# Kernel optimization log

Measured on AMD Instinct MI355X. Metric: run time of the kernel, lower is better.

## Reference

```python
import jax, jax.numpy as jnp
import numpy as np
import math

DIM = 1024
NUM_HEADS = 16
HEAD_DIM = DIM // NUM_HEADS
ROPE_BASE = 10000.0


def _rope_cos_sin(seq_len, head_dim, dtype):
    inv_freq = 1.0 / (ROPE_BASE ** (jnp.arange(0, head_dim, 2, dtype=jnp.float32) / head_dim))
    t = jnp.arange(seq_len, dtype=jnp.float32)
    freqs = jnp.einsum('i,j->ij', t, inv_freq)          # (S, head_dim/2)
    emb = jnp.concatenate([freqs, freqs], axis=-1)      # (S, head_dim)
    return jnp.cos(emb).astype(dtype), jnp.sin(emb).astype(dtype)


def _rotate_half(x):
    x1, x2 = jnp.split(x, 2, axis=-1)
    return jnp.concatenate([-x2, x1], axis=-1)


def setup_inputs() -> dict:
    key = jax.random.key(0)
    kx, kq, kk, kv, ko = jax.random.split(key, 5)
    B, S = 4, 2048
    scale = 1.0 / math.sqrt(DIM)
    x = jax.random.normal(kx, (B, S, DIM), dtype=jnp.float32)
    Wq = jax.random.normal(kq, (DIM, DIM), dtype=jnp.float32) * scale
    Wk = jax.random.normal(kk, (DIM, DIM), dtype=jnp.float32) * scale
    Wv = jax.random.normal(kv, (DIM, DIM), dtype=jnp.float32) * scale
    Wo = jax.random.normal(ko, (DIM, DIM), dtype=jnp.float32) * scale
    mask = jnp.tril(jnp.ones((S, S), dtype=jnp.int32))  # causal mask
    return {"x": x, "Wq": Wq, "Wk": Wk, "Wv": Wv, "Wo": Wo, "mask": mask}


def reference(x, Wq, Wk, Wv, Wo, mask):
    B, S, _ = x.shape
    # projections (nn.Linear: y = x @ W.T)
    def split_heads(t):
        return t.reshape(B, S, NUM_HEADS, HEAD_DIM).transpose(0, 2, 1, 3)  # (B,H,S,D)
    q = split_heads(x @ Wq.T)
    k = split_heads(x @ Wk.T)
    v = split_heads(x @ Wv.T)
    # RoPE
    cos, sin = _rope_cos_sin(S, HEAD_DIM, x.dtype)      # (S, D)
    cos = cos[None, None]; sin = sin[None, None]
    q = q * cos + _rotate_half(q) * sin
    k = k * cos + _rotate_half(k) * sin
    # attention
    scores = jnp.einsum('bhsd,bhtd->bhst', q, k) / math.sqrt(HEAD_DIM)
    neg_inf = jnp.asarray(-jnp.inf, dtype=scores.dtype)
    scores = jnp.where(mask[None, None] == 0, neg_inf, scores)
    attn = jax.nn.softmax(scores, axis=-1)
    out = jnp.einsum('bhst,bhtd->bhsd', attn, v)        # (B,H,S,D)
    out = out.transpose(0, 2, 1, 3).reshape(B, S, DIM)
    return out @ Wo.T
```

## Files before the change

kernel.cpp:

```cpp
#include <hip/hip_runtime.h>
#include <hip/hip_bf16.h>

#define BDIM 1024
#define NH 16
#define HD 64
#define BB 4
#define SS 2048
#define MTOT (BB*SS)
#define NT (SS/64)

typedef __bf16 bf16x8 __attribute__((ext_vector_type(8)));
typedef float f32x4 __attribute__((ext_vector_type(4)));

__device__ __forceinline__ unsigned short f2b(float f){
    __bf16 h = (__bf16)f;
    return __builtin_bit_cast(unsigned short, h);
}

__device__ __forceinline__ unsigned cvtpk(float lo, float hi){
    unsigned u;
    asm("v_cvt_pk_bf16_f32 %0, %1, %2" : "=v"(u) : "v"(lo), "v"(hi));
    return u;
}

__device__ __forceinline__ void ld16(const unsigned short* g, unsigned short* l){
    __builtin_amdgcn_global_load_lds(
        (const __attribute__((address_space(1))) unsigned int*)(const void*)g,
        (__attribute__((address_space(3))) unsigned int*)(void*)l, 16, 0, 0);
}

__global__ void setup_all(const float* __restrict__ x,
                          const float* __restrict__ Wq, const float* __restrict__ Wk,
                          const float* __restrict__ Wv, const float* __restrict__ Wo,
                          unsigned short* __restrict__ xb,
                          unsigned short* __restrict__ oq, unsigned short* __restrict__ ok,
                          unsigned short* __restrict__ ov, unsigned short* __restrict__ oo,
                          float2* __restrict__ rt){
    const int bid = blockIdx.x;
    const int tid = threadIdx.x;
    if (bid < 8192){
        int i = bid * 256 + tid;
        float4 v = ((const float4*)x)[i];
        ushort4 o;
        o.x = f2b(v.x); o.y = f2b(v.y); o.z = f2b(v.z); o.w = f2b(v.w);
        ((ushort4*)xb)[i] = o;
    } else if (bid < 12288){
        int idx = bid - 8192;
        int which = idx >> 10;
        const float* in = (which == 0) ? Wq : (which == 1) ? Wk : (which == 2) ? Wv : Wo;
        unsigned short* out = (which == 0) ? oq : (which == 1) ? ok : (which == 2) ? ov : oo;
        int i = (idx & 1023) * 256 + tid;
        float4 v = ((const float4*)in)[i];
        ushort4 o;
        o.x = f2b(v.x); o.y = f2b(v.y); o.z = f2b(v.z); o.w = f2b(v.w);
        ((ushort4*)out)[i] = o;
    } else {
        int i = (bid - 12288) * 256 + tid;
        int s = i >> 5, d = i & 31;
        float theta = (float)s * exp2f(-0.41524101186092029f * (float)d);
        float sn, c;
        sincosf(theta, &sn, &c);
        rt[i] = make_float2(c, sn);
    }
}

__device__ __forceinline__ void gemm_mainloop(
    const unsigned short* __restrict__ A,
    const unsigned short* __restrict__ Bw,
    unsigned short* At, unsigned short* Bt,
    f32x4 acc[4][4], int m0, int n0)
{
    const int tid  = threadIdx.x;
    const int lane = tid & 63;
    const int wave = tid >> 6;
    const int wr = wave >> 1, wc = wave & 1;
    const int lh = lane >> 4, ll = lane & 15;
    const int K = 1024;

    for (int k0 = 0; k0 < K; k0 += 64){
        #pragma unroll
        for (int c = 0; c < 4; ++c){
            int g   = c*256 + tid;
            int row = g >> 3;
            int off = (g & 7) * 8;
            int base = (c*256 + wave*64) * 8;
            ld16(A  + (size_t)(m0+row)*K + k0 + off, At + base);
            ld16(Bw + (size_t)(n0+row)*K + k0 + off, Bt + base);
        }
        __syncthreads();
        #pragma unroll
        for (int ks = 0; ks < 2; ++ks){
            bf16x8 af[4], bfr[4];
            #pragma unroll
            for (int i = 0; i < 4; ++i)
                af[i] = *(const bf16x8*)(At + (wr*64 + i*16 + ll)*64 + ks*32 + lh*8);
            #pragma unroll
            for (int j = 0; j < 4; ++j)
                bfr[j] = *(const bf16x8*)(Bt + (wc*64 + j*16 + ll)*64 + ks*32 + lh*8);
            #pragma unroll
            for (int i = 0; i < 4; ++i)
                #pragma unroll
                for (int j = 0; j < 4; ++j)
                    acc[i][j] = __builtin_amdgcn_mfma_f32_16x16x32_bf16(af[i], bfr[j], acc[i][j], 0, 0, 0);
        }
        __syncthreads();
    }
}

#define TILE_US 4096

__global__ __launch_bounds__(256, 4) void gemm_qkv(
    const unsigned short* __restrict__ Xb,
    const unsigned short* __restrict__ Wq,
    const unsigned short* __restrict__ Wk,
    const unsigned short* __restrict__ Wv,
    const float2* __restrict__ Rt,
    unsigned short* __restrict__ Qt,
    unsigned short* __restrict__ Kt,
    unsigned short* __restrict__ VTt)
{
    __shared__ alignas(16) unsigned short At[128*64];
    __shared__ alignas(16) unsigned short Bt[128*64];
    const int z = blockIdx.z;
    const unsigned short* Bw = (z == 0) ? Wq : (z == 1 ? Wk : Wv);
    const int m0 = blockIdx.y * 128, n0 = blockIdx.x * 128;
    f32x4 acc[4][4] = {};
    gemm_mainloop(Xb, Bw, At, Bt, acc, m0, n0);

    const int lane = threadIdx.x & 63;
    const int wave = threadIdx.x >> 6;
    const int wr = wave >> 1, wc = wave & 1;
    const int lh = lane >> 4, ll = lane & 15;
    const int h  = blockIdx.x*2 + wc;
    const int b  = m0 >> 11;
    const int bh = b*NH + h;

    if (z < 2){
        const float qs = (z == 0) ? 0.125f * 1.44269504f : 1.0f;
        unsigned short* C = (z == 0) ? Qt : Kt;
        #pragma unroll
        for (int i = 0; i < 4; ++i)
            #pragma unroll
            for (int r = 0; r < 4; ++r){
                int m = m0 + wr*64 + i*16 + lh*4 + r;
                int s = m & (SS-1);
                int kt = s >> 6;
                const float2* rowcs = Rt + (s << 5);
                size_t fb = ((size_t)(bh*NT + kt)*8 + i)*512 + (size_t)(lh*4 + r)*8;
                #pragma unroll
                for (int jl = 0; jl < 2; ++jl){
                    int d_lo = jl*16 + ll;
                    float2 cs = rowcs[d_lo];
                    float a_lo = acc[i][jl][r], a_hi = acc[i][jl+2][r];
                    float y_lo = (a_lo*cs.x - a_hi*cs.y) * qs;
                    float y_hi = (a_hi*cs.x + a_lo*cs.y) * qs;
                    size_t off = fb + (size_t)(jl*2 + (ll>>3))*128 + (ll&7);
                    C[off]        = f2b(y_lo);
                    C[off + 2048] = f2b(y_hi);
                }
            }
    } else {
        const int s0 = (m0 & (SS-1)) + wr*64;
        const int kt = s0 >> 6;
        #pragma unroll
        for (int i = 0; i < 4; ++i)
            #pragma unroll
            for (int j = 0; j < 4; ++j){
                unsigned short tmp[4];
                #pragma unroll
                for (int r = 0; r < 4; ++r)
                    tmp[r] = f2b(acc[i][j][r]);
                size_t off = ((size_t)(bh*NT + kt)*8 + (i>>1)*4 + j)*512
                           + (size_t)(((i&1)*2 + (lh>>1))*16 + ll)*8 + (lh&1)*4;
                *(uint2*)(VTt + off) = *(const uint2*)tmp;
            }
    }
}

__global__ __launch_bounds__(256, 4) void gemm_out(
    const unsigned short* __restrict__ Ab,
    const unsigned short* __restrict__ Wo,
    float* __restrict__ Cout)
{
    __shared__ alignas(16) unsigned short At[128*64];
    __shared__ alignas(16) unsigned short Bt[128*64];
    const int m0 = blockIdx.y * 128, n0 = blockIdx.x * 128;
    f32x4 acc[4][4] = {};
    gemm_mainloop(Ab, Wo, At, Bt, acc, m0, n0);

    const int lane = threadIdx.x & 63;
    const int wave = threadIdx.x >> 6;
    const int wr = wave >> 1, wc = wave & 1;
    const int lh = lane >> 4, ll = lane & 15;
    #pragma unroll
    for (int i = 0; i < 4; ++i)
        #pragma unroll
        for (int j = 0; j < 4; ++j)
            #pragma unroll
            for (int r = 0; r < 4; ++r){
                int m = m0 + wr*64 + i*16 + lh*4 + r;
                int n = n0 + wc*64 + j*16 + ll;
                Cout[(size_t)m*BDIM + n] = acc[i][j][r];
            }
}

__device__ __forceinline__ void attn_tile(
    const bf16x8 qf[2], bool diag, int ws, int lane, int lh, int ll,
    const unsigned short* Ksh, const unsigned short* Vsh,
    float& li, f32x4 o[4])
{
    f32x4 sc[4] = {};
    #pragma unroll
    for (int ks = 0; ks < 2; ++ks)
        #pragma unroll
        for (int j = 0; j < 4; ++j){
            bf16x8 kfr = *(const bf16x8*)(Ksh + (ks*4 + j)*512 + lane*8);
            sc[j] = __builtin_amdgcn_mfma_f32_16x16x32_bf16(kfr, qf[ks], sc[j], 0, 0, 0);
        }
    if (diag){
        int qrow = ws*16 + ll;
        #pragma unroll
        for (int j = 0; j < 4; ++j)
            #pragma unroll
            for (int r = 0; r < 4; ++r)
                if (j*16 + lh*4 + r > qrow) sc[j][r] = -1e30f;
    }
    #pragma unroll
    for (int j = 0; j < 4; ++j)
        #pragma unroll
        for (int r = 0; r < 4; ++r)
            sc[j][r] = exp2f(sc[j][r] - 28.0f);
    float s = 0.f;
    #pragma unroll
    for (int j = 0; j < 4; ++j)
        s += (sc[j][0] + sc[j][1]) + (sc[j][2] + sc[j][3]);
    li += s;
    #pragma unroll
    for (int ks = 0; ks < 2; ++ks){
        unsigned a = cvtpk(sc[2*ks][0],   sc[2*ks][1]);
        unsigned b = cvtpk(sc[2*ks+1][0], sc[2*ks+1][1]);
        unsigned c = cvtpk(sc[2*ks][2],   sc[2*ks][3]);
        unsigned d = cvtpk(sc[2*ks+1][2], sc[2*ks+1][3]);
        asm("v_permlane32_swap_b32 %0, %1" : "+v"(a), "+v"(b));
        asm("v_permlane16_swap_b32 %0, %1" : "+v"(a), "+v"(b));
        asm("v_permlane32_swap_b32 %0, %1" : "+v"(c), "+v"(d));
        asm("v_permlane16_swap_b32 %0, %1" : "+v"(c), "+v"(d));
        uint4 uu = make_uint4(a, c, b, d);
        bf16x8 pf = __builtin_bit_cast(bf16x8, uu);
        #pragma unroll
        for (int t = 0; t < 4; ++t){
            bf16x8 vf = *(const bf16x8*)(Vsh + (ks*4 + t)*512 + lane*8);
            o[t] = __builtin_amdgcn_mfma_f32_16x16x32_bf16(pf, vf, o[t], 0, 0, 0);
        }
    }
}

__device__ __forceinline__ void store_o(
    unsigned short* S, const f32x4 o[4], const float li[4],
    int lane, int lh, int ll, int q0w, int b, int h,
    unsigned short* __restrict__ Obuf)
{
    #pragma unroll
    for (int r = 0; r < 4; ++r){
        float inv = 1.0f / li[r];
        #pragma unroll
        for (int t = 0; t < 4; ++t)
            S[(lh*4 + r)*72 + t*16 + ll] = f2b(o[t][r] * inv);
    }
    int row = lane >> 2, c4 = (lane & 3) * 8;
    size_t rb = ((size_t)(b*SS + q0w + row))*BDIM + h*HD;
    *(uint4*)(Obuf + rb + c4)      = *(uint4*)(S + row*72 + c4);
    *(uint4*)(Obuf + rb + 32 + c4) = *(uint4*)(S + row*72 + 32 + c4);
}

__global__ __launch_bounds__(512, 4) void attn_kernel(
    const unsigned short* __restrict__ Qt,
    const unsigned short* __restrict__ Kt,
    const unsigned short* __restrict__ VTt,
    unsigned short* __restrict__ Obuf)
{
    __shared__ alignas(16) unsigned short Ksh[2][TILE_US];
    __shared__ alignas(16) unsigned short Vsh[2][TILE_US];
    __shared__ alignas(16) unsigned short Psh[8][16*72];

    const int tid  = threadIdx.x;
    const int lane = tid & 63;
    const int wave = tid >> 6;
    const int grp  = wave >> 2;
    const int ws   = wave & 3;
    const int lh = lane >> 4, ll = lane & 15;
    const int bx = blockIdx.x;
    const int bh = blockIdx.y;

    const int tS = (grp == 0) ? bx        : 15 - bx;
    const int tL = (grp == 0) ? NT-1 - bx : 16 + bx;
    const int ktMax = NT-1 - bx;

    const unsigned short* Qhf = Qt  + (size_t)bh * NT * TILE_US;
    const unsigned short* Khf = Kt  + (size_t)bh * NT * TILE_US;
    const unsigned short* Vhf = VTt + (size_t)bh * NT * TILE_US;

    bf16x8 qfS[2], qfL[2];
    #pragma unroll
    for (int ks = 0; ks < 2; ++ks){
        qfS[ks] = *(const bf16x8*)(Qhf + (size_t)(tS*8 + ks*4 + ws)*512 + lane*8);
        qfL[ks] = *(const bf16x8*)(Qhf + (size_t)(tL*8 + ks*4 + ws)*512 + lane*8);
    }

    f32x4 oS[4] = {}, oL[4] = {};
    float liS = 0.f, liL = 0.f;

    const int tb = tid * 8;

    {
        uint4 k0 = *(const uint4*)(Khf + tb);
        uint4 v0 = *(const uint4*)(Vhf + tb);
        *(uint4*)(&Ksh[0][0] + tb) = k0;
        *(uint4*)(&Vsh[0][0] + tb) = v0;
    }
    __syncthreads();

    int cur = 0;
    for (int kt = 0; kt <= ktMax; ++kt){
        uint4 kr, vr;
        if (kt < ktMax){
            size_t nb = (size_t)(kt + 1) * TILE_US + tb;
            kr = *(const uint4*)(Khf + nb);
            vr = *(const uint4*)(Vhf + nb);
        }
        if (kt <= tL)
            attn_tile(qfL, kt == tL, ws, lane, lh, ll, &Ksh[cur][0], &Vsh[cur][0], liL, oL);
        if (kt <= tS)
            attn_tile(qfS, kt == tS, ws, lane, lh, ll, &Ksh[cur][0], &Vsh[cur][0], liS, oS);
        if (kt < ktMax){
            *(uint4*)(&Ksh[cur^1][0] + tb) = kr;
            *(uint4*)(&Vsh[cur^1][0] + tb) = vr;
        }
        __syncthreads();
        cur ^= 1;
    }

    liS += __shfl_xor(liS, 16); liS += __shfl_xor(liS, 32);
    liL += __shfl_xor(liL, 16); liL += __shfl_xor(liL, 32);
    float livS[4], livL[4];
    #pragma unroll
    for (int r = 0; r < 4; ++r){
        livS[r] = __shfl(liS, lh*4 + r);
        livL[r] = __shfl(liL, lh*4 + r);
    }

    int b = bh >> 4, h = bh & 15;
    store_o(Psh[wave], oS, livS, lane, lh, ll, tS*64 + ws*16, b, h, Obuf);
    store_o(Psh[wave], oL, livL, lane, lh, ll, tL*64 + ws*16, b, h, Obuf);
}

extern "C" void kernel_launch(void* const* d_in, const int* in_sizes, int n_in,
                              void* d_out, int out_size, void* d_ws, size_t ws_size,
                              hipStream_t stream) {
    const float* x  = (const float*)d_in[0];
    const float* Wq = (const float*)d_in[1];
    const float* Wk = (const float*)d_in[2];
    const float* Wv = (const float*)d_in[3];
    const float* Wo = (const float*)d_in[4];

    char* w = (char*)d_ws;
    unsigned short* xb  = (unsigned short*)(w);
    unsigned short* wqb = (unsigned short*)(w + (16u  << 20));
    unsigned short* wkb = (unsigned short*)(w + (18u  << 20));
    unsigned short* wvb = (unsigned short*)(w + (20u  << 20));
    unsigned short* wob = (unsigned short*)(w + (22u  << 20));
    unsigned short* Qt  = (unsigned short*)(w + (24u  << 20));
    unsigned short* Kt  = (unsigned short*)(w + (40u  << 20));
    unsigned short* VTt = (unsigned short*)(w + (56u  << 20));
    unsigned short* Ob  = (unsigned short*)(w + (72u  << 20));
    float2*         Rt  = (float2*)(w + (88u << 20));

    setup_all<<<12544, 256, 0, stream>>>(x, Wq, Wk, Wv, Wo, xb, wqb, wkb, wvb, wob, Rt);

    gemm_qkv<<<dim3(8, 64, 3), 256, 0, stream>>>(xb, wqb, wkb, wvb, Rt, Qt, Kt, VTt);
    attn_kernel<<<dim3(8, 64), 512, 0, stream>>>(Qt, Kt, VTt, Ob);
    gemm_out<<<dim3(8, 64), 256, 0, stream>>>(Ob, wob, (float*)d_out);
}
```

Baseline: 275.1 us.

## Fuse Q/K/V projections into one GEMM sharing the X tile, add block swizzle

The QKV GEMM now computes all three projections in one block, loading the X tile once into shared memory and reusing it against Wq, Wk and Wv tiles. This cuts the X reads from global memory threefold and drops the z grid dimension. Three accumulator sets raise register pressure, so launch bounds go from 4 to 2 blocks per CU and shared memory grows to 64KB. A block-index swizzle is also added to both GEMMs to improve L2 locality. With fewer blocks (512) and lower occupancy, latency hiding may get worse.

```diff
diff --git a/kernel.cpp b/kernel.cpp
--- a/kernel.cpp
+++ b/kernel.cpp
@@ -64,52 +64,43 @@
     }
 }
 
-__device__ __forceinline__ void gemm_mainloop(
-    const unsigned short* __restrict__ A,
-    const unsigned short* __restrict__ Bw,
-    unsigned short* At, unsigned short* Bt,
-    f32x4 acc[4][4], int m0, int n0)
-{
-    const int tid  = threadIdx.x;
-    const int lane = tid & 63;
-    const int wave = tid >> 6;
-    const int wr = wave >> 1, wc = wave & 1;
-    const int lh = lane >> 4, ll = lane & 15;
-    const int K = 1024;
-
-    for (int k0 = 0; k0 < K; k0 += 64){
-        #pragma unroll
-        for (int c = 0; c < 4; ++c){
-            int g   = c*256 + tid;
-            int row = g >> 3;
-            int off = (g & 7) * 8;
-            int base = (c*256 + wave*64) * 8;
-            ld16(A  + (size_t)(m0+row)*K + k0 + off, At + base);
-            ld16(Bw + (size_t)(n0+row)*K + k0 + off, Bt + base);
-        }
-        __syncthreads();
-        #pragma unroll
-        for (int ks = 0; ks < 2; ++ks){
-            bf16x8 af[4], bfr[4];
-            #pragma unroll
-            for (int i = 0; i < 4; ++i)
-                af[i] = *(const bf16x8*)(At + (wr*64 + i*16 + ll)*64 + ks*32 + lh*8);
-            #pragma unroll
-            for (int j = 0; j < 4; ++j)
-                bfr[j] = *(const bf16x8*)(Bt + (wc*64 + j*16 + ll)*64 + ks*32 + lh*8);
-            #pragma unroll
-            for (int i = 0; i < 4; ++i)
-                #pragma unroll
-                for (int j = 0; j < 4; ++j)
-                    acc[i][j] = __builtin_amdgcn_mfma_f32_16x16x32_bf16(af[i], bfr[j], acc[i][j], 0, 0, 0);
-        }
-        __syncthreads();
-    }
-}
-
 #define TILE_US 4096
 
-__global__ __launch_bounds__(256, 4) void gemm_qkv(
+__device__ __forceinline__ void swz_xy(int& xs, int& ys){
+    int id = blockIdx.x + 8*blockIdx.y;
+    xs = id >> 6;
+    int t = id & 63;
+    ys = (t & 7)*8 + (t >> 3);
+}
+
+__device__ __forceinline__ void rope_store(
+    const f32x4 acc[4][4], float qs, unsigned short* __restrict__ C,
+    const float2* __restrict__ Rt, int m0, int bh, int wr, int lh, int ll)
+{
+    #pragma unroll
+    for (int i = 0; i < 4; ++i)
+        #pragma unroll
+        for (int r = 0; r < 4; ++r){
+            int m = m0 + wr*64 + i*16 + lh*4 + r;
+            int s = m & (SS-1);
+            int kt = s >> 6;
+            const float2* rowcs = Rt + (s << 5);
+            size_t fb = ((size_t)(bh*NT + kt)*8 + i)*512 + (size_t)(lh*4 + r)*8;
+            #pragma unroll
+            for (int jl = 0; jl < 2; ++jl){
+                int d_lo = jl*16 + ll;
+                float2 cs = rowcs[d_lo];
+                float a_lo = acc[i][jl][r], a_hi = acc[i][jl+2][r];
+                float y_lo = (a_lo*cs.x - a_hi*cs.y) * qs;
+                float y_hi = (a_hi*cs.x + a_lo*cs.y) * qs;
+                size_t off = fb + (size_t)(jl*2 + (ll>>3))*128 + (ll&7);
+                C[off]        = f2b(y_lo);
+                C[off + 2048] = f2b(y_hi);
+            }
+        }
+}
+
+__global__ __launch_bounds__(256, 2) void gemm_qkv(
     const unsigned short* __restrict__ Xb,
     const unsigned short* __restrict__ Wq,
     const unsigned short* __restrict__ Wk,
@@ -119,47 +110,88 @@
     unsigned short* __restrict__ Kt,
     unsigned short* __restrict__ VTt)
 {
-    __shared__ alignas(16) unsigned short At[128*64];
-    __shared__ alignas(16) unsigned short Bt[128*64];
-    const int z = blockIdx.z;
-    const unsigned short* Bw = (z == 0) ? Wq : (z == 1 ? Wk : Wv);
-    const int m0 = blockIdx.y * 128, n0 = blockIdx.x * 128;
-    f32x4 acc[4][4] = {};
-    gemm_mainloop(Xb, Bw, At, Bt, acc, m0, n0);
-
-    const int lane = threadIdx.x & 63;
-    const int wave = threadIdx.x >> 6;
+    __shared__ alignas(16) unsigned short At [128*64];
+    __shared__ alignas(16) unsigned short Bt0[128*64];
+    __shared__ alignas(16) unsigned short Bt1[128*64];
+    __shared__ alignas(16) unsigned short Bt2[128*64];
+
+    int xs, ys;
+    swz_xy(xs, ys);
+    const int m0 = ys*128, n0 = xs*128;
+
+    const int tid  = threadIdx.x;
+    const int lane = tid & 63;
+    const int wave = tid >> 6;
     const int wr = wave >> 1, wc = wave & 1;
     const int lh = lane >> 4, ll = lane & 15;
-    const int h  = blockIdx.x*2 + wc;
+    const int K = 1024;
+
+    f32x4 accq[4][4] = {}, acck[4][4] = {}, accv[4][4] = {};
+
+    for (int k0 = 0; k0 < K; k0 += 64){
+        #pragma unroll
+        for (int c = 0; c < 4; ++c){
+            int g   = c*256 + tid;
+            int row = g >> 3;
+            int off = (g & 7) * 8;
+            int base = (c*256 + wave*64) * 8;
+            ld16(Xb + (size_t)(m0+row)*K + k0 + off, At  + base);
+            ld16(Wq + (size_t)(n0+row)*K + k0 + off, Bt0 + base);
+            ld16(Wk + (size_t)(n0+row)*K + k0 + off, Bt1 + base);
+            ld16(Wv + (size_t)(n0+row)*K + k0 + off, Bt2 + base);
+        }
+        __syncthreads();
+        #pragma unroll
+        for (int ks = 0; ks < 2; ++ks){
+            bf16x8 af[4];
+            #pragma unroll
+            for (int i = 0; i < 4; ++i)
+                af[i] = *(const bf16x8*)(At + (wr*64 + i*16 + ll)*64 + ks*32 + lh*8);
+            {
+                bf16x8 b[4];
+                #pragma unroll
+                for (int j = 0; j < 4; ++j)
+                    b[j] = *(const bf16x8*)(Bt0 + (wc*64 + j*16 + ll)*64 + ks*32 + lh*8);
+                #pragma unroll
+                for (int i = 0; i < 4; ++i)
+                    #pragma unroll
+                    for (int j = 0; j < 4; ++j)
+                        accq[i][j] = __builtin_amdgcn_mfma_f32_16x16x32_bf16(af[i], b[j], accq[i][j], 0, 0, 0);
+            }
+            {
+                bf16x8 b[4];
+                #pragma unroll
+                for (int j = 0; j < 4; ++j)
+                    b[j] = *(const bf16x8*)(Bt1 + (wc*64 + j*16 + ll)*64 + ks*32 + lh*8);
+                #pragma unroll
+                for (int i = 0; i < 4; ++i)
+                    #pragma unroll
+                    for (int j = 0; j < 4; ++j)
+                        acck[i][j] = __builtin_amdgcn_mfma_f32_16x16x32_bf16(af[i], b[j], acck[i][j], 0, 0, 0);
+            }
+            {
+                bf16x8 b[4];
+                #pragma unroll
+                for (int j = 0; j < 4; ++j)
+                    b[j] = *(const bf16x8*)(Bt2 + (wc*64 + j*16 + ll)*64 + ks*32 + lh*8);
+                #pragma unroll
+                for (int i = 0; i < 4; ++i)
+                    #pragma unroll
+                    for (int j = 0; j < 4; ++j)
+                        accv[i][j] = __builtin_amdgcn_mfma_f32_16x16x32_bf16(af[i], b[j], accv[i][j], 0, 0, 0);
+            }
+        }
+        __syncthreads();
+    }
+
+    const int h  = xs*2 + wc;
     const int b  = m0 >> 11;
     const int bh = b*NH + h;
 
-    if (z < 2){
-        const float qs = (z == 0) ? 0.125f * 1.44269504f : 1.0f;
-        unsigned short* C = (z == 0) ? Qt : Kt;
-        #pragma unroll
-        for (int i = 0; i < 4; ++i)
-            #pragma unroll
-            for (int r = 0; r < 4; ++r){
-                int m = m0 + wr*64 + i*16 + lh*4 + r;
-                int s = m & (SS-1);
-                int kt = s >> 6;
-                const float2* rowcs = Rt + (s << 5);
-                size_t fb = ((size_t)(bh*NT + kt)*8 + i)*512 + (size_t)(lh*4 + r)*8;
-                #pragma unroll
-                for (int jl = 0; jl < 2; ++jl){
-                    int d_lo = jl*16 + ll;
-                    float2 cs = rowcs[d_lo];
-                    float a_lo = acc[i][jl][r], a_hi = acc[i][jl+2][r];
-                    float y_lo = (a_lo*cs.x - a_hi*cs.y) * qs;
-                    float y_hi = (a_hi*cs.x + a_lo*cs.y) * qs;
-                    size_t off = fb + (size_t)(jl*2 + (ll>>3))*128 + (ll&7);
-                    C[off]        = f2b(y_lo);
-                    C[off + 2048] = f2b(y_hi);
-                }
-            }
-    } else {
+    rope_store(accq, 0.125f * 1.44269504f, Qt, Rt, m0, bh, wr, lh, ll);
+    rope_store(acck, 1.0f,                 Kt, Rt, m0, bh, wr, lh, ll);
+
+    {
         const int s0 = (m0 & (SS-1)) + wr*64;
         const int kt = s0 >> 6;
         #pragma unroll
@@ -169,7 +201,7 @@
                 unsigned short tmp[4];
                 #pragma unroll
                 for (int r = 0; r < 4; ++r)
-                    tmp[r] = f2b(acc[i][j][r]);
+                    tmp[r] = f2b(accv[i][j][r]);
                 size_t off = ((size_t)(bh*NT + kt)*8 + (i>>1)*4 + j)*512
                            + (size_t)(((i&1)*2 + (lh>>1))*16 + ll)*8 + (lh&1)*4;
                 *(uint2*)(VTt + off) = *(const uint2*)tmp;
@@ -184,14 +216,47 @@
 {
     __shared__ alignas(16) unsigned short At[128*64];
     __shared__ alignas(16) unsigned short Bt[128*64];
-    const int m0 = blockIdx.y * 128, n0 = blockIdx.x * 128;
-    f32x4 acc[4][4] = {};
-    gemm_mainloop(Ab, Wo, At, Bt, acc, m0, n0);
-
-    const int lane = threadIdx.x & 63;
-    const int wave = threadIdx.x >> 6;
+    int xs, ys;
+    swz_xy(xs, ys);
+    const int m0 = ys * 128, n0 = xs * 128;
+
+    const int tid  = threadIdx.x;
+    const int lane = tid & 63;
+    const int wave = tid >> 6;
     const int wr = wave >> 1, wc = wave & 1;
     const int lh = lane >> 4, ll = lane & 15;
+    const int K = 1024;
+
+    f32x4 acc[4][4] = {};
+    for (int k0 = 0; k0 < K; k0 += 64){
+        #pragma unroll
+        for (int c = 0; c < 4; ++c){
+            int g   = c*256 + tid;
+            int row = g >> 3;
+            int off = (g & 7) * 8;
+            int base = (c*256 + wave*64) * 8;
+            ld16(Ab + (size_t)(m0+row)*K + k0 + off, At + base);
+            ld16(Wo + (size_t)(n0+row)*K + k0 + off, Bt + base);
+        }
+        __syncthreads();
+        #pragma unroll
+        for (int ks = 0; ks < 2; ++ks){
+            bf16x8 af[4], bfr[4];
+            #pragma unroll
+            for (int i = 0; i < 4; ++i)
+                af[i] = *(const bf16x8*)(At + (wr*64 + i*16 + ll)*64 + ks*32 + lh*8);
+            #pragma unroll
+            for (int j = 0; j < 4; ++j)
+                bfr[j] = *(const bf16x8*)(Bt + (wc*64 + j*16 + ll)*64 + ks*32 + lh*8);
+            #pragma unroll
+            for (int i = 0; i < 4; ++i)
+                #pragma unroll
+                for (int j = 0; j < 4; ++j)
+                    acc[i][j] = __builtin_amdgcn_mfma_f32_16x16x32_bf16(af[i], bfr[j], acc[i][j], 0, 0, 0);
+        }
+        __syncthreads();
+    }
+
     #pragma unroll
     for (int i = 0; i < 4; ++i)
         #pragma unroll
@@ -377,7 +442,7 @@
 
     setup_all<<<12544, 256, 0, stream>>>(x, Wq, Wk, Wv, Wo, xb, wqb, wkb, wvb, wob, Rt);
 
-    gemm_qkv<<<dim3(8, 64, 3), 256, 0, stream>>>(xb, wqb, wkb, wvb, Rt, Qt, Kt, VTt);
+    gemm_qkv<<<dim3(8, 64), 256, 0, stream>>>(xb, wqb, wkb, wvb, Rt, Qt, Kt, VTt);
     attn_kernel<<<dim3(8, 64), 512, 0, stream>>>(Qt, Kt, VTt, Ob);
     gemm_out<<<dim3(8, 64), 256, 0, stream>>>(Ob, wob, (float*)d_out);
 }
```

Measured after the change: 292.9 us. 1.06x slower.
